# Kernel optimization log

Hardware: AMD Instinct MI355X
Metric: run time of the kernel (lower is better)

The kernel has to match this reference:

```python
import jax, jax.numpy as jnp
import numpy as np

N_CUST, N_PROD, N_EDGES, EMBED_DIM, HIDDEN = 100000, 100000, 1000000, 64, 64


def setup_inputs() -> dict:
    key = jax.random.key(0)
    ks = jax.random.split(key, 8)
    D = EMBED_DIM
    return {
        "h_customer": jax.random.normal(ks[0], (N_CUST, D), dtype=jnp.float32),
        "h_product": jax.random.normal(ks[1], (N_PROD, D), dtype=jnp.float32),
        "src_idx": jax.random.randint(ks[2], (N_EDGES,), 0, N_CUST),
        "dst_idx": jax.random.randint(ks[3], (N_EDGES,), 0, N_PROD),
        "W1": jax.random.normal(ks[4], (2 * D + 1, HIDDEN), dtype=jnp.float32) * 0.05,
        "b1": jnp.zeros((HIDDEN,), dtype=jnp.float32),
        "W2": jax.random.normal(ks[5], (HIDDEN, 1), dtype=jnp.float32) * 0.05,
        "b2": jnp.zeros((1,), dtype=jnp.float32),
    }


def reference(h_customer, h_product, src_idx, dst_idx, W1, b1, W2, b2):
    # Per-edge gather of head/tail node embeddings: [E, D]
    heads = h_customer[src_idx]
    tails = h_product[dst_idx]

    # F.normalize(p=2, dim=-1), torch eps = 1e-12
    hn = heads / jnp.maximum(jnp.linalg.norm(heads, axis=-1, keepdims=True), 1e-12)
    tn = tails / jnp.maximum(jnp.linalg.norm(tails, axis=-1, keepdims=True), 1e-12)

    # cosine_similarity of already-normalized vectors, torch eps = 1e-8
    denom = jnp.maximum(
        jnp.linalg.norm(hn, axis=-1) * jnp.linalg.norm(tn, axis=-1), 1e-8
    )
    cos = jnp.sum(hn * tn, axis=-1) / denom  # [E]

    # concat(raw heads, raw tails, cosine) -> [E, 2D+1]
    cat = jnp.concatenate([heads, tails, cos[:, None]], axis=1)

    # small prediction MLP -> sigmoid ratings, [E, 1]
    x = jax.nn.relu(cat @ W1 + b1)
    ratings = jax.nn.sigmoid(x @ W2 + b2)
    return ratings
```

## Files before the change

### kernel.cpp

```cpp
#include <hip/hip_runtime.h>
#include <math.h>


typedef __attribute__((ext_vector_type(8))) short bf16x8;
typedef __attribute__((ext_vector_type(4))) float f32x4;
typedef __attribute__((ext_vector_type(2))) float float2_t;
typedef __attribute__((ext_vector_type(8))) unsigned short ushort8_t;
typedef __attribute__((ext_vector_type(4))) float float4_t;
typedef __attribute__((ext_vector_type(4))) unsigned int uint4_t;
typedef __attribute__((ext_vector_type(2))) unsigned int uint2_t;

#define T_STRIDE 72
#define P_STRIDE 72

__device__ __forceinline__ float bf2f(unsigned short u) {
    return __uint_as_float(((unsigned int)u) << 16);
}
__device__ __forceinline__ unsigned short f2bf(float f) {
    unsigned int x = __float_as_uint(f);
    return (unsigned short)((x + 0x7fffu + ((x >> 16) & 1u)) >> 16);
}

__global__ __launch_bounds__(256) void prep_w1(
    const float* __restrict__ W1, unsigned short* __restrict__ frag)
{
    int idx = blockIdx.x * 256 + threadIdx.x;
    if (idx >= 2 * 4 * 2 * 64 * 8) return;
    int j    = idx & 7;
    int lane = (idx >> 3) & 63;
    int ks   = (idx >> 9) & 1;
    int nt   = (idx >> 10) & 3;
    int half = (idx >> 12) & 1;
    int k   = ks * 32 + (lane >> 4) * 8 + j;
    int col = nt * 16 + (lane & 15);
    frag[idx] = f2bf(W1[(half * 64 + k) * 64 + col]);
}

__global__ __launch_bounds__(256) void node_fused(
    const float* __restrict__ hc, const float* __restrict__ hp,
    const unsigned short* __restrict__ w1frag, const float* __restrict__ b1,
    unsigned int* __restrict__ hnc, unsigned int* __restrict__ hnp,
    unsigned short* __restrict__ pcb, unsigned short* __restrict__ ppb,
    int nC, int nP, int blocksC)
{
    __shared__ unsigned short tile[64 * T_STRIDE];
    __shared__ unsigned short tile2[64 * P_STRIDE];

    int b = blockIdx.x;
    const float* h; unsigned int* hn; unsigned short* pj; int n, half;
    if (b < blocksC) { h = hc; hn = hnc; pj = pcb; n = nC; half = 0; }
    else { b -= blocksC; h = hp; hn = hnp; pj = ppb; n = nP; half = 1; }

    int node0 = b * 64;
    int nloc  = min(64, n - node0);
    int t     = threadIdx.x;
    int nl    = t >> 2, q = t & 3;

    if (nl < nloc) {
        const float* srcp = h + (long)(node0 + nl) * 64 + q * 16;
        float4_t v[4];
#pragma unroll
        for (int i = 0; i < 4; i++)
            v[i] = *reinterpret_cast<const float4_t*>(srcp + i * 4);

        float ss = 0.f;
#pragma unroll
        for (int i = 0; i < 4; i++)
#pragma unroll
            for (int j = 0; j < 4; j++) ss += v[i][j] * v[i][j];
        ss += __shfl_xor(ss, 1);
        ss += __shfl_xor(ss, 2);
        float inv = 1.f / fmaxf(sqrtf(ss), 1e-12f);

        uint4_t u8;
#pragma unroll
        for (int i = 0; i < 4; i++) {
            unsigned int d = __builtin_amdgcn_cvt_pk_fp8_f32(
                v[i][0] * inv, v[i][1] * inv, 0, false);
            d = __builtin_amdgcn_cvt_pk_fp8_f32(
                v[i][2] * inv, v[i][3] * inv, d, true);
            u8[i] = d;
        }
        *reinterpret_cast<uint4_t*>(hn + (long)(node0 + nl) * 16 + q * 4) = u8;

        ushort8_t u[2];
#pragma unroll
        for (int i = 0; i < 16; i++) u[i >> 3][i & 7] = f2bf(v[i >> 2][i & 3]);
        *reinterpret_cast<ushort8_t*>(&tile[nl * T_STRIDE + q * 16])     = u[0];
        *reinterpret_cast<ushort8_t*>(&tile[nl * T_STRIDE + q * 16 + 8]) = u[1];
    }
    __syncthreads();

    int wave = t >> 6, lane = t & 63;
    int m = lane & 15, quad = lane >> 4;
    if (wave * 16 < nloc) {
        bf16x8 a[2];
#pragma unroll
        for (int ks = 0; ks < 2; ks++)
            a[ks] = *reinterpret_cast<const bf16x8*>(
                &tile[(wave * 16 + m) * T_STRIDE + ks * 32 + quad * 8]);

        f32x4 acc[4];
#pragma unroll
        for (int nt = 0; nt < 4; nt++) acc[nt] = (f32x4){0.f, 0.f, 0.f, 0.f};
#pragma unroll
        for (int nt = 0; nt < 4; nt++)
#pragma unroll
            for (int ks = 0; ks < 2; ks++) {
                bf16x8 bf = *reinterpret_cast<const bf16x8*>(
                    &w1frag[(((half * 4 + nt) * 2 + ks) * 64 + lane) * 8]);
                acc[nt] = __builtin_amdgcn_mfma_f32_16x16x32_bf16(
                    a[ks], bf, acc[nt], 0, 0, 0);
            }
        if (half == 0) {
#pragma unroll
            for (int nt = 0; nt < 4; nt++) {
                float bb = b1[nt * 16 + m];
#pragma unroll
                for (int r = 0; r < 4; r++) acc[nt][r] += bb;
            }
        }
#pragma unroll
        for (int nt = 0; nt < 4; nt++)
#pragma unroll
            for (int r = 0; r < 4; r++)
                tile2[(wave * 16 + quad * 4 + r) * P_STRIDE + nt * 16 + m]
                    = f2bf(acc[nt][r]);
    }
    __syncthreads();

    if (nl < nloc) {
        ushort8_t p0 = *reinterpret_cast<ushort8_t*>(&tile2[nl * P_STRIDE + q * 16]);
        ushort8_t p1 = *reinterpret_cast<ushort8_t*>(&tile2[nl * P_STRIDE + q * 16 + 8]);
        unsigned short* dstp = pj + (long)(node0 + nl) * 64 + q * 16;
        *reinterpret_cast<ushort8_t*>(dstp)     = p0;
        *reinterpret_cast<ushort8_t*>(dstp + 8) = p1;
    }
}

__global__ __launch_bounds__(256) void edge_mlp(
    const unsigned int* __restrict__ hnc, const unsigned int* __restrict__ hnp,
    const unsigned short* __restrict__ pc, const unsigned short* __restrict__ pp,
    const int* __restrict__ src, const int* __restrict__ dst,
    const float* __restrict__ W1, const float* __restrict__ W2,
    const float* __restrict__ b2, float* __restrict__ out, int nE)
{
    int lane = threadIdx.x & 63;
    int sub  = lane >> 3;
    int g    = lane & 7;
    int d0   = g * 8;
    int e    = ((blockIdx.x * 256 + threadIdx.x) >> 6) * 8 + sub;
    bool valid = e < nE;
    int s = valid ? src[e] : 0;
    int t = valid ? dst[e] : 0;

    float4_t w1a = *reinterpret_cast<const float4_t*>(W1 + 128 * 64 + d0);
    float4_t w1b = *reinterpret_cast<const float4_t*>(W1 + 128 * 64 + d0 + 4);
    float4_t w2a = *reinterpret_cast<const float4_t*>(W2 + d0);
    float4_t w2b = *reinterpret_cast<const float4_t*>(W2 + d0 + 4);
    float b2v = b2[0];

    uint2_t hs = *reinterpret_cast<const uint2_t*>(hnc + (long)s * 16 + g * 2);
    uint2_t ht = *reinterpret_cast<const uint2_t*>(hnp + (long)t * 16 + g * 2);
    ushort8_t ps8 = *reinterpret_cast<const ushort8_t*>(pc + (long)s * 64 + d0);
    ushort8_t pt8 = *reinterpret_cast<const ushort8_t*>(pp + (long)t * 64 + d0);

    float hsv[8], htv[8];
#pragma unroll
    for (int w = 0; w < 2; w++) {
        float2_t lo = __builtin_amdgcn_cvt_pk_f32_fp8((int)hs[w], false);
        float2_t hi = __builtin_amdgcn_cvt_pk_f32_fp8((int)hs[w], true);
        hsv[w*4+0] = lo[0]; hsv[w*4+1] = lo[1]; hsv[w*4+2] = hi[0]; hsv[w*4+3] = hi[1];
        float2_t lo2 = __builtin_amdgcn_cvt_pk_f32_fp8((int)ht[w], false);
        float2_t hi2 = __builtin_amdgcn_cvt_pk_f32_fp8((int)ht[w], true);
        htv[w*4+0] = lo2[0]; htv[w*4+1] = lo2[1]; htv[w*4+2] = hi2[0]; htv[w*4+3] = hi2[1];
    }

    float dot = 0.f;
#pragma unroll
    for (int i = 0; i < 8; i++) dot += hsv[i] * htv[i];
    dot += __shfl_xor(dot, 1);
    dot += __shfl_xor(dot, 2);
    dot += __shfl_xor(dot, 4);
    float cosv = dot;

    float w1l[8] = {w1a[0], w1a[1], w1a[2], w1a[3], w1b[0], w1b[1], w1b[2], w1b[3]};
    float w2v[8] = {w2a[0], w2a[1], w2a[2], w2a[3], w2b[0], w2b[1], w2b[2], w2b[3]};
    float p = 0.f;
#pragma unroll
    for (int i = 0; i < 8; i++) {
        float x = bf2f(ps8[i]) + bf2f(pt8[i]) + cosv * w1l[i];
        x = fmaxf(x, 0.f);
        p += x * w2v[i];
    }
    p += __shfl_xor(p, 1);
    p += __shfl_xor(p, 2);
    p += __shfl_xor(p, 4);

    if (valid && g == 0)
        out[e] = 1.f / (1.f + expf(-(p + b2v)));
}

extern "C" void kernel_launch(void* const* d_in, const int* in_sizes, int n_in,
                              void* d_out, int out_size, void* d_ws, size_t ws_size,
                              hipStream_t stream) {
    const float* h_c = (const float*)d_in[0];
    const float* h_p = (const float*)d_in[1];
    const int*   src = (const int*)d_in[2];
    const int*   dst = (const int*)d_in[3];
    const float* W1  = (const float*)d_in[4];
    const float* b1  = (const float*)d_in[5];
    const float* W2  = (const float*)d_in[6];
    const float* b2  = (const float*)d_in[7];
    float* out = (float*)d_out;

    int nC = in_sizes[0] / 64;
    int nP = in_sizes[1] / 64;
    int nE = in_sizes[2];

    char* ws = (char*)d_ws;
    size_t off = 0;
    auto carve = [&](size_t bytes) {
        void* p = ws + off;
        off = (off + bytes + 255) & ~(size_t)255;
        return p;
    };
    unsigned int*   hnc = (unsigned int*)carve((size_t)nC * 64);
    unsigned int*   hnp = (unsigned int*)carve((size_t)nP * 64);
    unsigned short* pcb = (unsigned short*)carve((size_t)nC * 64 * 2);
    unsigned short* ppb = (unsigned short*)carve((size_t)nP * 64 * 2);
    unsigned short* w1f = (unsigned short*)carve((size_t)16384 * 2);

    prep_w1<<<64, 256, 0, stream>>>(W1, w1f);

    int blocksC = (nC + 63) / 64, blocksP = (nP + 63) / 64;
    node_fused<<<blocksC + blocksP, 256, 0, stream>>>(
        h_c, h_p, w1f, b1, hnc, hnp, pcb, ppb, nC, nP, blocksC);

    edge_mlp<<<(nE + 31) / 32, 256, 0, stream>>>(
        hnc, hnp, pcb, ppb, src, dst, W1, W2, b2, out, nE);
}
```

Baseline: 173.4 us.

## Load node rows directly into MFMA layout and widen per-lane edge work

In the node kernel, each lane now loads its fp32 row slice straight into the MFMA A-fragment layout. This removes the bf16 staging tile in LDS and one block barrier, at the cost of less coalesced global reads. In the edge kernel, each edge is handled by 4 lanes instead of 8, so each lane issues wider 16-byte gathers and 16 edges are processed per wave. That halves the grid and shortens the shuffle reductions, but raises per-thread register use.

Measured after the change: 174.9 us. Within noise of the previous version (+0.8%).

```diff
diff --git a/kernel.cpp b/kernel.cpp
--- a/kernel.cpp
+++ b/kernel.cpp
@@ -10,7 +10,6 @@
 typedef __attribute__((ext_vector_type(4))) unsigned int uint4_t;
 typedef __attribute__((ext_vector_type(2))) unsigned int uint2_t;
 
-#define T_STRIDE 72
 #define P_STRIDE 72
 
 __device__ __forceinline__ float bf2f(unsigned short u) {
@@ -43,7 +42,6 @@
     unsigned short* __restrict__ pcb, unsigned short* __restrict__ ppb,
     int nC, int nP, int blocksC)
 {
-    __shared__ unsigned short tile[64 * T_STRIDE];
     __shared__ unsigned short tile2[64 * P_STRIDE];
 
     int b = blockIdx.x;
@@ -54,51 +52,51 @@
     int node0 = b * 64;
     int nloc  = min(64, n - node0);
     int t     = threadIdx.x;
-    int nl    = t >> 2, q = t & 3;
-
-    if (nl < nloc) {
-        const float* srcp = h + (long)(node0 + nl) * 64 + q * 16;
-        float4_t v[4];
-#pragma unroll
-        for (int i = 0; i < 4; i++)
-            v[i] = *reinterpret_cast<const float4_t*>(srcp + i * 4);
+    int wave  = t >> 6, lane = t & 63;
+    int m = lane & 15, quad = lane >> 4;
+
+    if (wave * 16 < nloc) {
+        int row = node0 + wave * 16 + m;
+        float4_t f[2][2];
+#pragma unroll
+        for (int ks = 0; ks < 2; ks++) {
+            const float* srcp = h + (long)row * 64 + ks * 32 + quad * 8;
+            f[ks][0] = *reinterpret_cast<const float4_t*>(srcp);
+            f[ks][1] = *reinterpret_cast<const float4_t*>(srcp + 4);
+        }
 
         float ss = 0.f;
 #pragma unroll
-        for (int i = 0; i < 4; i++)
-#pragma unroll
-            for (int j = 0; j < 4; j++) ss += v[i][j] * v[i][j];
-        ss += __shfl_xor(ss, 1);
-        ss += __shfl_xor(ss, 2);
+        for (int ks = 0; ks < 2; ks++)
+#pragma unroll
+            for (int i = 0; i < 2; i++)
+#pragma unroll
+                for (int j = 0; j < 4; j++) ss += f[ks][i][j] * f[ks][i][j];
+        ss += __shfl_xor(ss, 16);
+        ss += __shfl_xor(ss, 32);
         float inv = 1.f / fmaxf(sqrtf(ss), 1e-12f);
 
-        uint4_t u8;
-#pragma unroll
-        for (int i = 0; i < 4; i++) {
-            unsigned int d = __builtin_amdgcn_cvt_pk_fp8_f32(
-                v[i][0] * inv, v[i][1] * inv, 0, false);
-            d = __builtin_amdgcn_cvt_pk_fp8_f32(
-                v[i][2] * inv, v[i][3] * inv, d, true);
-            u8[i] = d;
+#pragma unroll
+        for (int ks = 0; ks < 2; ks++) {
+            uint2_t u8;
+#pragma unroll
+            for (int i = 0; i < 2; i++) {
+                unsigned int d = __builtin_amdgcn_cvt_pk_fp8_f32(
+                    f[ks][i][0] * inv, f[ks][i][1] * inv, 0, false);
+                d = __builtin_amdgcn_cvt_pk_fp8_f32(
+                    f[ks][i][2] * inv, f[ks][i][3] * inv, d, true);
+                u8[i] = d;
+            }
+            *reinterpret_cast<uint2_t*>(
+                reinterpret_cast<char*>(hn) + (long)row * 64 + ks * 32 + quad * 8) = u8;
         }
-        *reinterpret_cast<uint4_t*>(hn + (long)(node0 + nl) * 16 + q * 4) = u8;
-
-        ushort8_t u[2];
-#pragma unroll
-        for (int i = 0; i < 16; i++) u[i >> 3][i & 7] = f2bf(v[i >> 2][i & 3]);
-        *reinterpret_cast<ushort8_t*>(&tile[nl * T_STRIDE + q * 16])     = u[0];
-        *reinterpret_cast<ushort8_t*>(&tile[nl * T_STRIDE + q * 16 + 8]) = u[1];
-    }
-    __syncthreads();
-
-    int wave = t >> 6, lane = t & 63;
-    int m = lane & 15, quad = lane >> 4;
-    if (wave * 16 < nloc) {
+
         bf16x8 a[2];
 #pragma unroll
         for (int ks = 0; ks < 2; ks++)
-            a[ks] = *reinterpret_cast<const bf16x8*>(
-                &tile[(wave * 16 + m) * T_STRIDE + ks * 32 + quad * 8]);
+#pragma unroll
+            for (int i = 0; i < 8; i++)
+                a[ks][i] = (short)f2bf(f[ks][i >> 2][i & 3]);
 
         f32x4 acc[4];
 #pragma unroll
@@ -129,6 +127,7 @@
     }
     __syncthreads();
 
+    int nl = t >> 2, q = t & 3;
     if (nl < nloc) {
         ushort8_t p0 = *reinterpret_cast<ushort8_t*>(&tile2[nl * P_STRIDE + q * 16]);
         ushort8_t p1 = *reinterpret_cast<ushort8_t*>(&tile2[nl * P_STRIDE + q * 16 + 8]);
@@ -146,56 +145,53 @@
     const float* __restrict__ b2, float* __restrict__ out, int nE)
 {
     int lane = threadIdx.x & 63;
-    int sub  = lane >> 3;
-    int g    = lane & 7;
-    int d0   = g * 8;
-    int e    = ((blockIdx.x * 256 + threadIdx.x) >> 6) * 8 + sub;
+    int sub  = lane >> 2;
+    int g    = lane & 3;
+    int d0   = g * 16;
+    int e    = ((blockIdx.x * 256 + threadIdx.x) >> 6) * 16 + sub;
     bool valid = e < nE;
     int s = valid ? src[e] : 0;
     int t = valid ? dst[e] : 0;
 
-    float4_t w1a = *reinterpret_cast<const float4_t*>(W1 + 128 * 64 + d0);
-    float4_t w1b = *reinterpret_cast<const float4_t*>(W1 + 128 * 64 + d0 + 4);
-    float4_t w2a = *reinterpret_cast<const float4_t*>(W2 + d0);
-    float4_t w2b = *reinterpret_cast<const float4_t*>(W2 + d0 + 4);
+    uint4_t hs = *reinterpret_cast<const uint4_t*>(hnc + (long)s * 16 + g * 4);
+    uint4_t ht = *reinterpret_cast<const uint4_t*>(hnp + (long)t * 16 + g * 4);
+    ushort8_t ps0 = *reinterpret_cast<const ushort8_t*>(pc + (long)s * 64 + d0);
+    ushort8_t ps1 = *reinterpret_cast<const ushort8_t*>(pc + (long)s * 64 + d0 + 8);
+    ushort8_t pt0 = *reinterpret_cast<const ushort8_t*>(pp + (long)t * 64 + d0);
+    ushort8_t pt1 = *reinterpret_cast<const ushort8_t*>(pp + (long)t * 64 + d0 + 8);
+
+    float4_t w1v[4], w2v[4];
+#pragma unroll
+    for (int i = 0; i < 4; i++) {
+        w1v[i] = *reinterpret_cast<const float4_t*>(W1 + 128 * 64 + d0 + i * 4);
+        w2v[i] = *reinterpret_cast<const float4_t*>(W2 + d0 + i * 4);
+    }
     float b2v = b2[0];
 
-    uint2_t hs = *reinterpret_cast<const uint2_t*>(hnc + (long)s * 16 + g * 2);
-    uint2_t ht = *reinterpret_cast<const uint2_t*>(hnp + (long)t * 16 + g * 2);
-    ushort8_t ps8 = *reinterpret_cast<const ushort8_t*>(pc + (long)s * 64 + d0);
-    ushort8_t pt8 = *reinterpret_cast<const ushort8_t*>(pp + (long)t * 64 + d0);
-
-    float hsv[8], htv[8];
-#pragma unroll
-    for (int w = 0; w < 2; w++) {
-        float2_t lo = __builtin_amdgcn_cvt_pk_f32_fp8((int)hs[w], false);
-        float2_t hi = __builtin_amdgcn_cvt_pk_f32_fp8((int)hs[w], true);
-        hsv[w*4+0] = lo[0]; hsv[w*4+1] = lo[1]; hsv[w*4+2] = hi[0]; hsv[w*4+3] = hi[1];
-        float2_t lo2 = __builtin_amdgcn_cvt_pk_f32_fp8((int)ht[w], false);
-        float2_t hi2 = __builtin_amdgcn_cvt_pk_f32_fp8((int)ht[w], true);
-        htv[w*4+0] = lo2[0]; htv[w*4+1] = lo2[1]; htv[w*4+2] = hi2[0]; htv[w*4+3] = hi2[1];
-    }
-
     float dot = 0.f;
 #pragma unroll
-    for (int i = 0; i < 8; i++) dot += hsv[i] * htv[i];
+    for (int w = 0; w < 4; w++) {
+        float2_t alo = __builtin_amdgcn_cvt_pk_f32_fp8((int)hs[w], false);
+        float2_t ahi = __builtin_amdgcn_cvt_pk_f32_fp8((int)hs[w], true);
+        float2_t blo = __builtin_amdgcn_cvt_pk_f32_fp8((int)ht[w], false);
+        float2_t bhi = __builtin_amdgcn_cvt_pk_f32_fp8((int)ht[w], true);
+        dot += alo[0] * blo[0] + alo[1] * blo[1] + ahi[0] * bhi[0] + ahi[1] * bhi[1];
+    }
     dot += __shfl_xor(dot, 1);
     dot += __shfl_xor(dot, 2);
-    dot += __shfl_xor(dot, 4);
     float cosv = dot;
 
-    float w1l[8] = {w1a[0], w1a[1], w1a[2], w1a[3], w1b[0], w1b[1], w1b[2], w1b[3]};
-    float w2v[8] = {w2a[0], w2a[1], w2a[2], w2a[3], w2b[0], w2b[1], w2b[2], w2b[3]};
     float p = 0.f;
 #pragma unroll
-    for (int i = 0; i < 8; i++) {
-        float x = bf2f(ps8[i]) + bf2f(pt8[i]) + cosv * w1l[i];
+    for (int i = 0; i < 16; i++) {
+        float pcv = bf2f(i < 8 ? ps0[i] : ps1[i - 8]);
+        float ppv = bf2f(i < 8 ? pt0[i] : pt1[i - 8]);
+        float x = pcv + ppv + cosv * w1v[i >> 2][i & 3];
         x = fmaxf(x, 0.f);
-        p += x * w2v[i];
+        p += x * w2v[i >> 2][i & 3];
     }
     p += __shfl_xor(p, 1);
     p += __shfl_xor(p, 2);
-    p += __shfl_xor(p, 4);
 
     if (valid && g == 0)
         out[e] = 1.f / (1.f + expf(-(p + b2v)));
@@ -237,6 +233,6 @@
     node_fused<<<blocksC + blocksP, 256, 0, stream>>>(
         h_c, h_p, w1f, b1, hnc, hnp, pcb, ppb, nC, nP, blocksC);
 
-    edge_mlp<<<(nE + 31) / 32, 256, 0, stream>>>(
+    edge_mlp<<<(nE + 63) / 64, 256, 0, stream>>>(
         hnc, hnp, pcb, ppb, src, dst, W1, W2, b2, out, nE);
 }
```
